# Kernel optimization log

Measured on AMD Instinct MI355X. Metric: run time of the kernel, lower is better.

Reference implementation:

```python
import jax, jax.numpy as jnp
import numpy as np

L, H, NH, V, T, B, K = 12, 768, 12, 30522, 512, 4, 21
DH = H // NH
INV_SQRT_DH = 1.0 / float(np.sqrt(DH))
NEG = -1e4  # BERT additive mask value
LN_EPS = 1e-12


def _ln(x, g, b):
    m = x.mean(-1, keepdims=True)
    v = jnp.var(x, axis=-1, keepdims=True)
    return (x - m) * jax.lax.rsqrt(v + LN_EPS) * g + b


def _encoder(input_ids, attention_mask, word_emb, pos_emb, tok_emb, emb_g, emb_b,
             Wqkv, bqkv, Wo, bo, ln1_g, ln1_b, W1, b1, W2, b2, ln2_g, ln2_b):
    Bv, Tv = input_ids.shape
    h = word_emb[input_ids] + pos_emb[None, :Tv] + tok_emb[0]  # token_type_ids = 0
    h = _ln(h, emb_g, emb_b)
    bias = (1.0 - attention_mask[:, None, None, :].astype(h.dtype)) * NEG  # [B,1,1,T]

    def layer(h, xs):
        wqkv, bq, wo, bo_, g1, b1_, w1, bb1, w2, bb2, g2, b2_ = xs
        qkv = h @ wqkv + bq  # [B,T,3H]
        q, k, v = jnp.split(qkv, 3, axis=-1)
        def hd(x):
            return x.reshape(Bv, Tv, NH, DH).transpose(0, 2, 1, 3)
        q, k, v = hd(q), hd(k), hd(v)
        scores = jnp.einsum('bhqd,bhkd->bhqk', q, k) * INV_SQRT_DH + bias
        ctx = jnp.einsum('bhqk,bhkd->bhqd', jax.nn.softmax(scores, axis=-1), v)
        ctx = ctx.transpose(0, 2, 1, 3).reshape(Bv, Tv, H)
        h = _ln(h + ctx @ wo + bo_, g1, b1_)  # post-LN (BERT)
        ff = jax.nn.gelu(h @ w1 + bb1, approximate=False) @ w2 + bb2
        h = _ln(h + ff, g2, b2_)
        return h, None

    h, _ = jax.lax.scan(layer, h, (Wqkv, bqkv, Wo, bo, ln1_g, ln1_b, W1, b1, W2, b2, ln2_g, ln2_b))
    return h


def _crf_nll(emissions, tags, mask, start, end, trans):
    # emissions [B,T,K], tags [B,T] int, mask [B,T] bool; torchcrf reduction='mean'
    Bv, Tv, Kv = emissions.shape
    maskf = mask.astype(emissions.dtype)
    # numerator: score of the gold path
    num = start[tags[:, 0]] + emissions[jnp.arange(Bv), 0, tags[:, 0]]
    em_t = jnp.take_along_axis(emissions, tags[..., None], axis=-1)[..., 0]  # [B,T]
    tr_t = trans[tags[:, :-1], tags[:, 1:]]  # [B,T-1]
    num = num + jnp.sum((tr_t + em_t[:, 1:]) * maskf[:, 1:], axis=1)
    last_idx = mask.sum(axis=1).astype(jnp.int32) - 1
    last_tag = jnp.take_along_axis(tags, last_idx[:, None], axis=1)[:, 0]
    num = num + end[last_tag]
    # denominator: forward algorithm (logsumexp recursion over time)
    alpha0 = start[None, :] + emissions[:, 0]  # [B,K]

    def step(alpha, xs):
        em, m = xs  # em [B,K], m [B] bool
        nxt = jax.scipy.special.logsumexp(alpha[:, :, None] + trans[None] + em[:, None, :], axis=1)
        return jnp.where(m[:, None], nxt, alpha), None

    alpha, _ = jax.lax.scan(step, alpha0, (emissions[:, 1:].transpose(1, 0, 2), mask[:, 1:].T))
    den = jax.scipy.special.logsumexp(alpha + end[None, :], axis=1)
    return -(num - den).mean()


def _viterbi(emissions, mask, start, end, trans):
    # Returns [B,T] int32 best paths; padded tail repeats the last valid tag.
    Bv, Tv, Kv = emissions.shape
    score0 = start[None, :] + emissions[:, 0]
    ident = jnp.broadcast_to(jnp.arange(Kv), (Bv, Kv))

    def step(score, xs):
        em, m = xs
        cand = score[:, :, None] + trans[None]  # [B,K_prev,K_next]
        idx = jnp.where(m[:, None], jnp.argmax(cand, axis=1), ident)
        nxt = jnp.max(cand, axis=1) + em
        return jnp.where(m[:, None], nxt, score), idx

    score, hist = jax.lax.scan(step, score0, (emissions[:, 1:].transpose(1, 0, 2), mask[:, 1:].T))
    last = jnp.argmax(score + end[None, :], axis=1)  # [B]

    def back(nxt_tag, idx):
        prev = jnp.take_along_axis(idx, nxt_tag[:, None], axis=1)[:, 0]
        return prev, nxt_tag

    tag0, rest = jax.lax.scan(back, last, hist, reverse=True)  # rest[i] = tag at t=i+1
    return jnp.concatenate([tag0[None], rest], axis=0).T.astype(jnp.int32)


def setup_inputs():
    key = jax.random.key(0)
    ks = jax.random.split(key, 16)
    s = 0.02

    def n(k, shape):
        return (s * jax.random.normal(k, shape)).astype(jnp.float32)

    def u(k, shape):
        return jax.random.uniform(k, shape, minval=-0.1, maxval=0.1).astype(jnp.float32)

    p = {}
    p['input_ids'] = jax.random.randint(ks[0], (B, T), 0, V)
    lengths = jax.random.randint(ks[1], (B,), T // 2, T + 1)
    p['attention_mask'] = (jnp.arange(T)[None, :] < lengths[:, None]).astype(jnp.int32)
    p['valid_mask'] = p['attention_mask']
    p['labels'] = jax.random.randint(ks[2], (B, T), 0, K)
    p['word_emb'] = n(ks[3], (V, H))
    p['pos_emb'] = n(ks[4], (T, H))
    p['tok_emb'] = n(ks[5], (2, H))
    p['emb_g'] = jnp.ones((H,), jnp.float32)
    p['emb_b'] = jnp.zeros((H,), jnp.float32)
    p['Wqkv'] = n(ks[6], (L, H, 3 * H))
    p['bqkv'] = jnp.zeros((L, 3 * H), jnp.float32)
    p['Wo'] = n(ks[7], (L, H, H))
    p['bo'] = jnp.zeros((L, H), jnp.float32)
    p['ln1_g'] = jnp.ones((L, H), jnp.float32)
    p['ln1_b'] = jnp.zeros((L, H), jnp.float32)
    p['W1'] = n(ks[8], (L, H, 4 * H))
    p['b1'] = jnp.zeros((L, 4 * H), jnp.float32)
    p['W2'] = n(ks[9], (L, 4 * H, H))
    p['b2'] = jnp.zeros((L, H), jnp.float32)
    p['ln2_g'] = jnp.ones((L, H), jnp.float32)
    p['ln2_b'] = jnp.zeros((L, H), jnp.float32)
    p['Wc'] = n(ks[10], (H, K))
    p['bc'] = jnp.zeros((K,), jnp.float32)
    p['crf_start'] = u(ks[11], (K,))
    p['crf_end'] = u(ks[12], (K,))
    p['crf_trans'] = u(ks[13], (K, K))
    return p


def reference(input_ids, attention_mask, valid_mask, labels,
              word_emb, pos_emb, tok_emb, emb_g, emb_b,
              Wqkv, bqkv, Wo, bo, ln1_g, ln1_b, W1, b1, W2, b2, ln2_g, ln2_b,
              Wc, bc, crf_start, crf_end, crf_trans):
    h = _encoder(input_ids, attention_mask, word_emb, pos_emb, tok_emb, emb_g, emb_b,
                 Wqkv, bqkv, Wo, bo, ln1_g, ln1_b, W1, b1, W2, b2, ln2_g, ln2_b)
    emissions = h @ Wc + bc  # dropout is identity in eval/reference mode
    mask = attention_mask.astype(bool)
    nll = _crf_nll(emissions, labels, mask, crf_start, crf_end, crf_trans)
    decoded = _viterbi(emissions, mask, crf_start, crf_end, crf_trans)
    return nll, decoded
```

## Files before the change

### kernel.cpp

```cpp
#include <hip/hip_runtime.h>
#include <math.h>

constexpr int NLAYER = 12;
constexpr int H = 768;
constexpr int NH = 12;
constexpr int DH = 64;
constexpr int T = 512;
constexpr int B = 4;
constexpr int K = 21;
constexpr int BT = B * T;
constexpr float NEGB = -10000.0f;
constexpr float LNEPS = 1e-12f;
constexpr float INV_SQRT_DH = 0.125f;

typedef __attribute__((ext_vector_type(8))) short bf16x8;
typedef __attribute__((ext_vector_type(4))) float f32x4;
typedef __attribute__((ext_vector_type(4))) unsigned short u16x4;

#define WAIT_VMCNT(n) asm volatile("s_waitcnt vmcnt(" #n ")")

__device__ __forceinline__ float wave_sum_f(float v) {
#pragma unroll
  for (int off = 32; off > 0; off >>= 1) v += __shfl_xor(v, off);
  return v;
}
__device__ __forceinline__ int wave_sum_i(int v) {
#pragma unroll
  for (int off = 32; off > 0; off >>= 1) v += __shfl_xor(v, off);
  return v;
}
__device__ __forceinline__ float readlane_f(float v, int i) {
  return __uint_as_float(__builtin_amdgcn_readlane(__float_as_uint(v), i));
}
__device__ __forceinline__ unsigned short f32_bf16_rn(float x) {
  unsigned int u = __float_as_uint(x);
  u += 0x7fffu + ((u >> 16) & 1u);
  return (unsigned short)(u >> 16);
}
__device__ __forceinline__ void split_bf16(float x, unsigned short& h, unsigned short& l) {
  h = f32_bf16_rn(x);
  float hf = __uint_as_float((unsigned int)h << 16);
  l = f32_bf16_rn(x - hf);
}
__device__ __forceinline__ void block_reduce_sum2(float& s, float& q) {
  __shared__ float red[8];
  s = wave_sum_f(s);
  q = wave_sum_f(q);
  int lane = threadIdx.x & 63, wid = threadIdx.x >> 6;
  if (lane == 0) { red[wid] = s; red[4 + wid] = q; }
  __syncthreads();
  s = red[0] + red[1] + red[2] + red[3];
  q = red[4] + red[5] + red[6] + red[7];
}

__global__ __launch_bounds__(256) void embed_ln_kernel(
    const int* __restrict__ ids, const float* __restrict__ wemb,
    const float* __restrict__ pemb, const float* __restrict__ temb,
    const float* __restrict__ g, const float* __restrict__ bta,
    float* __restrict__ h, unsigned short* __restrict__ hh,
    unsigned short* __restrict__ hl) {
  int row = blockIdx.x;
  int t = row % T;
  int id = ids[row];
  const float* wp = wemb + (size_t)id * H;
  const float* pp = pemb + (size_t)t * H;
  float x[3];
  float s = 0.f, q = 0.f;
#pragma unroll
  for (int i = 0; i < 3; i++) {
    int c = threadIdx.x + i * 256;
    x[i] = wp[c] + pp[c] + temb[c];
    s += x[i];
    q += x[i] * x[i];
  }
  block_reduce_sum2(s, q);
  float mean = s * (1.0f / H);
  float var = q * (1.0f / H) - mean * mean;
  float inv = rsqrtf(var + LNEPS);
#pragma unroll
  for (int i = 0; i < 3; i++) {
    int c = threadIdx.x + i * 256;
    float y = (x[i] - mean) * inv * g[c] + bta[c];
    h[(size_t)row * H + c] = y;
    unsigned short yh, yl;
    split_bf16(y, yh, yl);
    hh[(size_t)row * H + c] = yh;
    hl[(size_t)row * H + c] = yl;
  }
}

__global__ __launch_bounds__(256) void add_ln_kernel(
    float* __restrict__ h, const float* __restrict__ add,
    const float* __restrict__ g, const float* __restrict__ bta,
    unsigned short* __restrict__ hh, unsigned short* __restrict__ hl) {
  int row = blockIdx.x;
  size_t base = (size_t)row * H;
  float x[3];
  float s = 0.f, q = 0.f;
#pragma unroll
  for (int i = 0; i < 3; i++) {
    int c = threadIdx.x + i * 256;
    x[i] = h[base + c] + add[base + c];
    s += x[i];
    q += x[i] * x[i];
  }
  block_reduce_sum2(s, q);
  float mean = s * (1.0f / H);
  float var = q * (1.0f / H) - mean * mean;
  float inv = rsqrtf(var + LNEPS);
#pragma unroll
  for (int i = 0; i < 3; i++) {
    int c = threadIdx.x + i * 256;
    float y = (x[i] - mean) * inv * g[c] + bta[c];
    h[base + c] = y;
    unsigned short yh, yl;
    split_bf16(y, yh, yl);
    hh[base + c] = yh;
    hl[base + c] = yl;
  }
}

__global__ __launch_bounds__(256) void wconv_kernel(
    const float* __restrict__ w0, const float* __restrict__ w1,
    const float* __restrict__ w2, const float* __restrict__ w3,
    unsigned short* __restrict__ Wth, unsigned short* __restrict__ Wtl) {
  __shared__ float tile[32][33];
  int bid = blockIdx.x;
  const float* src;
  int Kd, N, tk, tn;
  size_t off;
  if (bid < 1728) {
    src = w0; Kd = 768; N = 2304; tk = bid / 72; tn = bid % 72; off = 0;
  } else if (bid < 2304) {
    int t2 = bid - 1728; src = w1; Kd = 768; N = 768; tk = t2 / 24; tn = t2 % 24;
    off = 1769472;
  } else if (bid < 4608) {
    int t2 = bid - 2304; src = w2; Kd = 768; N = 3072; tk = t2 / 96; tn = t2 % 96;
    off = 2359296;
  } else {
    int t2 = bid - 4608; src = w3; Kd = 3072; N = 768; tk = t2 / 24; tn = t2 % 24;
    off = 4718592;
  }
  int tid = threadIdx.x;
  int k0 = tk * 32, n0 = tn * 32;
  int r = tid >> 3, c = (tid & 7) * 4;
  float4 v = *(const float4*)(src + (size_t)(k0 + r) * N + n0 + c);
  tile[r][c + 0] = v.x; tile[r][c + 1] = v.y; tile[r][c + 2] = v.z; tile[r][c + 3] = v.w;
  __syncthreads();
  u16x4 hv, lv;
#pragma unroll
  for (int q2 = 0; q2 < 4; q2++) {
    unsigned short sh, sl;
    split_bf16(tile[c + q2][r], sh, sl);
    hv[q2] = sh; lv[q2] = sl;
  }
  size_t dst = off + (size_t)(n0 + r) * Kd + k0 + c;
  *(u16x4*)(Wth + dst) = hv;
  *(u16x4*)(Wtl + dst) = lv;
}

template <int BN, bool GELU, bool SPLITOUT>
__global__ __launch_bounds__(256) void gemm_bf3_kernel(
    const unsigned short* __restrict__ Ah, const unsigned short* __restrict__ Al,
    const unsigned short* __restrict__ Wth, const unsigned short* __restrict__ Wtl,
    const float* __restrict__ bias, float* __restrict__ C,
    unsigned short* __restrict__ Ch, unsigned short* __restrict__ Cl,
    int N, int Kd) {
  constexpr int WN = BN / 2;
  constexpr int FN = WN / 16;
  constexpr int AW = 128 * 32;
  constexpr int WW = BN * 32;
  constexpr int DBS = 2 * AW + 2 * WW;
  __shared__ short lds_s[2 * DBS];
  int tid = threadIdx.x;
  int lane = tid & 63, wid = tid >> 6;
  int wr = wid >> 1, wc = wid & 1;
  int bm = blockIdx.y * 128, bn = blockIdx.x * BN;
  f32x4 acc[4][FN] = {};
  int lrow = lane >> 2, lslot = lane & 3;

  const unsigned short* sbase;
  int rowbase, ldsoff, nchunks;
  if (wid == 0)      { sbase = Ah;  rowbase = bm; ldsoff = 0;            nchunks = 8; }
  else if (wid == 1) { sbase = Al;  rowbase = bm; ldsoff = AW;           nchunks = 8; }
  else if (wid == 2) { sbase = Wth; rowbase = bn; ldsoff = 2 * AW;       nchunks = BN / 16; }
  else               { sbase = Wtl; rowbase = bn; ldsoff = 2 * AW + WW;  nchunks = BN / 16; }

  const unsigned short* srcbase = sbase + (size_t)(rowbase + lrow) * Kd + lslot * 8;

  auto STAGE = [&](int db, int k0) {
#pragma unroll
    for (int c = 0; c < 8; c++) {
      if (c < nchunks) {
        const unsigned short* src = srcbase + (size_t)(c * 16) * Kd + k0;
        char* dst = ((char*)lds_s) + (db * DBS + ldsoff) * 2 + c * 1024 + lane * 16;
        __builtin_amdgcn_global_load_lds(
            (const __attribute__((address_space(1))) void*)src,
            (__attribute__((address_space(3))) void*)dst, 16, 0, 0);
      }
    }
  };

  const int NT = Kd / 32;
  STAGE(0, 0);
  for (int kt = 0; kt < NT; kt++) {
    int cur = kt & 1;
    bool more = (kt + 1 < NT);
    if (more) STAGE(cur ^ 1, (kt + 1) * 32);
    if (more) {
      if (BN == 128 || wid < 2) { WAIT_VMCNT(8); } else { WAIT_VMCNT(4); }
    } else {
      WAIT_VMCNT(0);
    }
    __builtin_amdgcn_s_barrier();
    __builtin_amdgcn_sched_barrier(0);

    int lr = lane & 15, lg = lane >> 4;
    int cb = cur * DBS;
    bf16x8 af_h[4], af_l[4], wf_h[FN], wf_l[FN];
#pragma unroll
    for (int i = 0; i < 4; i++) {
      int e = (wr * 64 + i * 16 + lr) * 32 + lg * 8;
      af_h[i] = *(const bf16x8*)&lds_s[cb + e];
      af_l[i] = *(const bf16x8*)&lds_s[cb + AW + e];
    }
#pragma unroll
    for (int j = 0; j < FN; j++) {
      int e = (wc * WN + j * 16 + lr) * 32 + lg * 8;
      wf_h[j] = *(const bf16x8*)&lds_s[cb + 2 * AW + e];
      wf_l[j] = *(const bf16x8*)&lds_s[cb + 2 * AW + WW + e];
    }
#pragma unroll
    for (int i = 0; i < 4; i++)
#pragma unroll
      for (int j = 0; j < FN; j++) {
        acc[i][j] = __builtin_amdgcn_mfma_f32_16x16x32_bf16(af_h[i], wf_h[j], acc[i][j], 0, 0, 0);
        acc[i][j] = __builtin_amdgcn_mfma_f32_16x16x32_bf16(af_l[i], wf_h[j], acc[i][j], 0, 0, 0);
        acc[i][j] = __builtin_amdgcn_mfma_f32_16x16x32_bf16(af_h[i], wf_l[j], acc[i][j], 0, 0, 0);
      }
    asm volatile("s_waitcnt lgkmcnt(0)");
    __builtin_amdgcn_sched_barrier(0);
    __builtin_amdgcn_s_barrier();
    __builtin_amdgcn_sched_barrier(0);
  }

  int lr = lane & 15, lg = lane >> 4;
#pragma unroll
  for (int i = 0; i < 4; i++) {
#pragma unroll
    for (int j = 0; j < FN; j++) {
      int row = bm + wr * 64 + i * 16 + lg * 4;
      int col = bn + wc * WN + j * 16 + lr;
      float bv = bias[col];
#pragma unroll
      for (int r = 0; r < 4; r++) {
        float v = acc[i][j][r] + bv;
        if (GELU) v = 0.5f * v * (1.0f + erff(v * 0.70710678118654752f));
        if (SPLITOUT) {
          unsigned short sh, sl;
          split_bf16(v, sh, sl);
          Ch[(size_t)(row + r) * N + col] = sh;
          Cl[(size_t)(row + r) * N + col] = sl;
        } else {
          C[(size_t)(row + r) * N + col] = v;
        }
      }
    }
  }
}

__global__ __launch_bounds__(256) void qk_kernel(
    const float* __restrict__ qkv, const int* __restrict__ mask,
    float* __restrict__ S) {
  int bh = blockIdx.z;
  int b = bh / NH, hh = bh % NH;
  int i0 = blockIdx.y * 64, j0 = blockIdx.x * 64;
  __shared__ float Qs[64][64];
  __shared__ float Ks[64][64];
  int tid = threadIdx.x;
  int r = tid >> 2;
  int cseg = (tid & 3) * 16;
  const float* qbase = qkv + (size_t)(b * T + i0 + r) * (3 * H) + hh * DH;
  const float* kbase = qkv + (size_t)(b * T + j0 + r) * (3 * H) + H + hh * DH;
#pragma unroll
  for (int ss = 0; ss < 4; ss++) {
    int c = cseg + ss * 4;
    float4 qa = *(const float4*)(qbase + c);
    float4 ka = *(const float4*)(kbase + c);
    Qs[c + 0][r] = qa.x; Qs[c + 1][r] = qa.y; Qs[c + 2][r] = qa.z; Qs[c + 3][r] = qa.w;
    Ks[c + 0][r] = ka.x; Ks[c + 1][r] = ka.y; Ks[c + 2][r] = ka.z; Ks[c + 3][r] = ka.w;
  }
  __syncthreads();
  int tx = tid & 15, ty = tid >> 4;
  float acc[4][4] = {};
#pragma unroll 4
  for (int d = 0; d < 64; d++) {
    float a_[4], b_[4];
    *(float4*)a_ = *(const float4*)&Qs[d][ty * 4];
    *(float4*)b_ = *(const float4*)&Ks[d][tx * 4];
#pragma unroll
    for (int i = 0; i < 4; i++)
#pragma unroll
      for (int j = 0; j < 4; j++)
        acc[i][j] = fmaf(a_[i], b_[j], acc[i][j]);
  }
  float bj[4];
#pragma unroll
  for (int q = 0; q < 4; q++)
    bj[q] = (1.0f - (float)mask[b * T + j0 + tx * 4 + q]) * NEGB;
#pragma unroll
  for (int i = 0; i < 4; i++) {
    int gi = i0 + ty * 4 + i;
    int gj = j0 + tx * 4;
    float4 o;
    o.x = acc[i][0] * INV_SQRT_DH + bj[0];
    o.y = acc[i][1] * INV_SQRT_DH + bj[1];
    o.z = acc[i][2] * INV_SQRT_DH + bj[2];
    o.w = acc[i][3] * INV_SQRT_DH + bj[3];
    *(float4*)(S + ((size_t)bh * T + gi) * T + gj) = o;
  }
}

__global__ __launch_bounds__(128) void softmax_kernel(float* __restrict__ S) {
  size_t row = blockIdx.x;
  float* p = S + row * T;
  int tid = threadIdx.x;
  float4 v = *(float4*)(p + tid * 4);
  float m = fmaxf(fmaxf(v.x, v.y), fmaxf(v.z, v.w));
#pragma unroll
  for (int off = 32; off > 0; off >>= 1) m = fmaxf(m, __shfl_xor(m, off));
  __shared__ float redm[2];
  __shared__ float reds[2];
  int wid = tid >> 6;
  if ((tid & 63) == 0) redm[wid] = m;
  __syncthreads();
  m = fmaxf(redm[0], redm[1]);
  v.x = __expf(v.x - m);
  v.y = __expf(v.y - m);
  v.z = __expf(v.z - m);
  v.w = __expf(v.w - m);
  float s = v.x + v.y + v.z + v.w;
  s = wave_sum_f(s);
  if ((tid & 63) == 0) reds[wid] = s;
  __syncthreads();
  s = reds[0] + reds[1];
  float inv = 1.0f / s;
  v.x *= inv; v.y *= inv; v.z *= inv; v.w *= inv;
  *(float4*)(p + tid * 4) = v;
}

__global__ __launch_bounds__(256) void pv_kernel(
    const float* __restrict__ S, const float* __restrict__ qkv,
    unsigned short* __restrict__ cth, unsigned short* __restrict__ ctl) {
  int bh = blockIdx.y;
  int b = bh / NH, hh = bh % NH;
  int i0 = blockIdx.x * 64;
  __shared__ float Ps[64][68];
  __shared__ float Vs[64][64];
  int tid = threadIdx.x;
  int r = tid >> 2;
  int cseg = (tid & 3) * 16;
  int tx = tid & 15, ty = tid >> 4;
  float acc[4][4] = {};
  const float* srow = S + ((size_t)bh * T + i0 + r) * T;
  const float* vbase = qkv + (size_t)(b * T) * (3 * H) + 2 * H + hh * DH;
  for (int k0 = 0; k0 < T; k0 += 64) {
    __syncthreads();
#pragma unroll
    for (int ss = 0; ss < 4; ss++) {
      int c = cseg + ss * 4;
      *(float4*)&Ps[r][c] = *(const float4*)(srow + k0 + c);
      *(float4*)&Vs[r][c] = *(const float4*)(vbase + (size_t)(k0 + r) * (3 * H) + c);
    }
    __syncthreads();
#pragma unroll
    for (int kk = 0; kk < 64; kk += 4) {
      float p_[4][4], v_[4][4];
#pragma unroll
      for (int i = 0; i < 4; i++)
        *(float4*)p_[i] = *(const float4*)&Ps[ty * 4 + i][kk];
#pragma unroll
      for (int s = 0; s < 4; s++)
        *(float4*)v_[s] = *(const float4*)&Vs[kk + s][tx * 4];
#pragma unroll
      for (int i = 0; i < 4; i++)
#pragma unroll
        for (int s = 0; s < 4; s++)
#pragma unroll
          for (int j = 0; j < 4; j++)
            acc[i][j] = fmaf(p_[i][s], v_[s][j], acc[i][j]);
    }
  }
#pragma unroll
  for (int i = 0; i < 4; i++) {
    int gi = i0 + ty * 4 + i;
    size_t idx = (size_t)(b * T + gi) * H + hh * DH + tx * 4;
    u16x4 hv, lv;
#pragma unroll
    for (int j = 0; j < 4; j++) {
      unsigned short sh, sl;
      split_bf16(acc[i][j], sh, sl);
      hv[j] = sh; lv[j] = sl;
    }
    *(u16x4*)(cth + idx) = hv;
    *(u16x4*)(ctl + idx) = lv;
  }
}

__global__ __launch_bounds__(256) void classifier_kernel(
    const float* __restrict__ h, const float* __restrict__ Wc,
    const float* __restrict__ bc, float* __restrict__ em) {
  int id = blockIdx.x * 256 + threadIdx.x;
  if (id >= BT * K) return;
  int row = id / K, k = id % K;
  float acc = bc[k];
  const float* hr = h + (size_t)row * H;
  for (int d = 0; d < H; d++) acc = fmaf(hr[d], Wc[d * K + k], acc);
  em[id] = acc;
}

#define MRG(vo, io, va, ia, vb, ib) \
  float vo = ((vb) > (va)) ? (vb) : (va); \
  int io = ((vb) > (va)) ? (ib) : (ia);

__global__ __launch_bounds__(64) void crf_fused_kernel(
    const float* __restrict__ em, const int* __restrict__ labels,
    const int* __restrict__ mask, const float* __restrict__ start,
    const float* __restrict__ endv, const float* __restrict__ trans,
    float* __restrict__ parts, float* __restrict__ outdec) {
  __shared__ float em_s[T * K];
  __shared__ int mask_s[T];
  __shared__ unsigned char hist_s[(T - 1) * K];
  __shared__ float sc_s[32];
  int b = blockIdx.x & 3;
  int role = blockIdx.x >> 2;
  int j = threadIdx.x;
  const float* eb = em + (size_t)b * T * K;
  for (int i = j; i < T * K / 4; i += 64)
    ((float4*)em_s)[i] = ((const float4*)eb)[i];
  for (int i = j; i < T; i += 64) mask_s[i] = mask[b * T + i];
  __syncthreads();
  bool act = (j < K);
  float tr[K];
#pragma unroll
  for (int i = 0; i < K; i++) tr[i] = act ? trans[i * K + j] : 0.f;

  if (role == 0) {
    const int* tb = labels + b * T;
    float numloc = 0.f;
    int cnt = 0;
    for (int t = j; t < T; t += 64) {
      cnt += mask_s[t];
      if (t >= 1 && mask_s[t]) {
        int tp = tb[t - 1], tc = tb[t];
        numloc += trans[tp * K + tc] + em_s[t * K + tc];
      }
    }
    float num = wave_sum_f(numloc);
    int cnttot = wave_sum_i(cnt);
    float etr[K];
#pragma unroll
    for (int i = 0; i < K; i++) etr[i] = __expf(tr[i]);
    float alpha = act ? (start[j] + em_s[j]) : 0.f;
    for (int t = 1; t < T; t++) {
      if (!mask_s[t]) continue;
      float m0 = readlane_f(alpha, 0);
      float ee = __expf(alpha - m0);
      float e0 = readlane_f(ee, 0),  e1 = readlane_f(ee, 1),  e2 = readlane_f(ee, 2);
      float e3 = readlane_f(ee, 3),  e4 = readlane_f(ee, 4),  e5 = readlane_f(ee, 5);
      float e6 = readlane_f(ee, 6),  e7 = readlane_f(ee, 7),  e8 = readlane_f(ee, 8);
      float e9 = readlane_f(ee, 9),  e10 = readlane_f(ee, 10), e11 = readlane_f(ee, 11);
      float e12 = readlane_f(ee, 12), e13 = readlane_f(ee, 13), e14 = readlane_f(ee, 14);
      float e15 = readlane_f(ee, 15), e16 = readlane_f(ee, 16), e17 = readlane_f(ee, 17);
      float e18 = readlane_f(ee, 18), e19 = readlane_f(ee, 19), e20 = readlane_f(ee, 20);
      float a0 = fmaf(e16, etr[16], fmaf(e12, etr[12], fmaf(e8, etr[8],  fmaf(e4, etr[4], e0 * etr[0]))));
      float a1 = fmaf(e17, etr[17], fmaf(e13, etr[13], fmaf(e9, etr[9],  fmaf(e5, etr[5], e1 * etr[1]))));
      float a2 = fmaf(e18, etr[18], fmaf(e14, etr[14], fmaf(e10, etr[10], fmaf(e6, etr[6], e2 * etr[2]))));
      float a3 = fmaf(e19, etr[19], fmaf(e15, etr[15], fmaf(e11, etr[11], fmaf(e7, etr[7], e3 * etr[3]))));
      float ssum = fmaf(e20, etr[20], (a0 + a1) + (a2 + a3));
      float nxt = __logf(ssum) + m0 + (act ? em_s[t * K + j] : 0.f);
      if (act) alpha = nxt;
    }
    float aj = act ? (alpha + endv[j]) : -3.0e38f;
    float mm = aj;
#pragma unroll
    for (int off = 32; off > 0; off >>= 1) mm = fmaxf(mm, __shfl_xor(mm, off));
    float e2v = act ? __expf(aj - mm) : 0.f;
    float s2 = wave_sum_f(e2v);
    float den = __logf(s2) + mm;
    if (j == 0) {
      int tag0 = tb[0];
      int lastidx = cnttot - 1;
      float numtot = num + start[tag0] + em_s[tag0] + endv[tb[lastidx]];
      parts[b] = numtot - den;
    }
  } else {
    float score = act ? (start[j] + em_s[j]) : 0.f;
    for (int t = 1; t < T; t++) {
      int mk = mask_s[t];
      if (mk) {
        float c0 = readlane_f(score, 0) + tr[0],   c1 = readlane_f(score, 1) + tr[1];
        float c2 = readlane_f(score, 2) + tr[2],   c3 = readlane_f(score, 3) + tr[3];
        float c4 = readlane_f(score, 4) + tr[4],   c5 = readlane_f(score, 5) + tr[5];
        float c6 = readlane_f(score, 6) + tr[6],   c7 = readlane_f(score, 7) + tr[7];
        float c8 = readlane_f(score, 8) + tr[8],   c9 = readlane_f(score, 9) + tr[9];
        float c10 = readlane_f(score, 10) + tr[10], c11 = readlane_f(score, 11) + tr[11];
        float c12 = readlane_f(score, 12) + tr[12], c13 = readlane_f(score, 13) + tr[13];
        float c14 = readlane_f(score, 14) + tr[14], c15 = readlane_f(score, 15) + tr[15];
        float c16 = readlane_f(score, 16) + tr[16], c17 = readlane_f(score, 17) + tr[17];
        float c18 = readlane_f(score, 18) + tr[18], c19 = readlane_f(score, 19) + tr[19];
        float c20 = readlane_f(score, 20) + tr[20];
        MRG(m0v, m0i, c0, 0, c1, 1)
        MRG(m1v, m1i, c2, 2, c3, 3)
        MRG(m2v, m2i, c4, 4, c5, 5)
        MRG(m3v, m3i, c6, 6, c7, 7)
        MRG(m4v, m4i, c8, 8, c9, 9)
        MRG(m5v, m5i, c10, 10, c11, 11)
        MRG(m6v, m6i, c12, 12, c13, 13)
        MRG(m7v, m7i, c14, 14, c15, 15)
        MRG(m8v, m8i, c16, 16, c17, 17)
        MRG(m9v, m9i, c18, 18, c19, 19)
        MRG(p0v, p0i, m0v, m0i, m1v, m1i)
        MRG(p1v, p1i, m2v, m2i, m3v, m3i)
        MRG(p2v, p2i, m4v, m4i, m5v, m5i)
        MRG(p3v, p3i, m6v, m6i, m7v, m7i)
        MRG(p4v, p4i, m8v, m8i, m9v, m9i)
        MRG(r0v, r0i, p0v, p0i, p1v, p1i)
        MRG(r1v, r1i, p2v, p2i, p3v, p3i)
        MRG(r2v, r2i, p4v, p4i, c20, 20)
        MRG(s0v, s0i, r0v, r0i, r1v, r1i)
        MRG(fv, fi, s0v, s0i, r2v, r2i)
        if (act) {
          hist_s[(t - 1) * K + j] = (unsigned char)fi;
          score = fv + em_s[t * K + j];
        }
      } else if (act) {
        hist_s[(t - 1) * K + j] = (unsigned char)j;
      }
    }
    if (act) sc_s[j] = score + endv[j];
    __syncthreads();
    if (j == 0) {
      float best = -3.0e38f;
      int cur = 0;
#pragma unroll
      for (int i = 0; i < K; i++)
        if (sc_s[i] > best) { best = sc_s[i]; cur = i; }
      outdec[b * T + (T - 1)] = (float)cur;
      for (int t = T - 1; t >= 1; t--) {
        cur = hist_s[(t - 1) * K + cur];
        outdec[b * T + (t - 1)] = (float)cur;
      }
    }
  }
}

__global__ void nll_final_kernel(const float* __restrict__ parts,
                                 float* __restrict__ out) {
  out[0] = -0.25f * (parts[0] + parts[1] + parts[2] + parts[3]);
}

extern "C" void kernel_launch(void* const* d_in, const int* in_sizes, int n_in,
                              void* d_out, int out_size, void* d_ws, size_t ws_size,
                              hipStream_t stream) {
  (void)in_sizes; (void)n_in; (void)out_size; (void)ws_size;
  const int* ids    = (const int*)d_in[0];
  const int* amask  = (const int*)d_in[1];
  const int* labels = (const int*)d_in[3];
  const float* wemb = (const float*)d_in[4];
  const float* pemb = (const float*)d_in[5];
  const float* temb = (const float*)d_in[6];
  const float* eg   = (const float*)d_in[7];
  const float* ebta = (const float*)d_in[8];
  const float* Wqkv = (const float*)d_in[9];
  const float* bqkv = (const float*)d_in[10];
  const float* Wo   = (const float*)d_in[11];
  const float* bo   = (const float*)d_in[12];
  const float* ln1g = (const float*)d_in[13];
  const float* ln1b = (const float*)d_in[14];
  const float* W1   = (const float*)d_in[15];
  const float* b1   = (const float*)d_in[16];
  const float* W2   = (const float*)d_in[17];
  const float* b2   = (const float*)d_in[18];
  const float* ln2g = (const float*)d_in[19];
  const float* ln2b = (const float*)d_in[20];
  const float* Wc   = (const float*)d_in[21];
  const float* bc   = (const float*)d_in[22];
  const float* cst  = (const float*)d_in[23];
  const float* cen  = (const float*)d_in[24];
  const float* ctr  = (const float*)d_in[25];
  float* out = (float*)d_out;

  float* ws = (float*)d_ws;
  float* h    = ws;
  unsigned short* hh = (unsigned short*)(h + 1572864);
  unsigned short* hl = (unsigned short*)(h + 1572864 + 786432);
  float* qkv  = h + 1572864 + 786432 * 2;
  unsigned short* cth = (unsigned short*)(qkv + 4718592);
  unsigned short* ctl = (unsigned short*)(qkv + 4718592 + 786432);
  float* tmp  = qkv + 4718592 + 786432 * 2;
  float* big  = tmp + 1572864;
  unsigned short* gh = (unsigned short*)(big + 12582912);
  unsigned short* gl = (unsigned short*)(big + 12582912 + 3145728);
  unsigned short* Wth = (unsigned short*)(big + 12582912 + 3145728 * 2);
  unsigned short* Wtl = (unsigned short*)(big + 12582912 + 3145728 * 2 + 3538944);
  float* em   = big + 12582912 + 3145728 * 2 + 3538944 * 2;
  float* parts = em + 43008;

  embed_ln_kernel<<<BT, 256, 0, stream>>>(ids, wemb, pemb, temb, eg, ebta, h, hh, hl);

  for (int l = 0; l < NLAYER; l++) {
    const float* bqkv_l = bqkv + (size_t)l * 3 * H;
    const float* bo_l   = bo + (size_t)l * H;
    const float* b1_l   = b1 + (size_t)l * 4 * H;
    const float* b2_l   = b2 + (size_t)l * H;

    wconv_kernel<<<6912, 256, 0, stream>>>(
        Wqkv + (size_t)l * H * 3 * H, Wo + (size_t)l * H * H,
        W1 + (size_t)l * H * 4 * H, W2 + (size_t)l * 4 * H * H, Wth, Wtl);

    gemm_bf3_kernel<128, false, false><<<dim3(18, 16), 256, 0, stream>>>(
        hh, hl, Wth, Wtl, bqkv_l, qkv, nullptr, nullptr, 3 * H, H);
    qk_kernel<<<dim3(T / 64, T / 64, B * NH), 256, 0, stream>>>(qkv, amask, big);
    softmax_kernel<<<B * NH * T, 128, 0, stream>>>(big);
    pv_kernel<<<dim3(T / 64, B * NH), 256, 0, stream>>>(big, qkv, cth, ctl);
    gemm_bf3_kernel<64, false, false><<<dim3(12, 16), 256, 0, stream>>>(
        cth, ctl, Wth + 1769472, Wtl + 1769472, bo_l, tmp, nullptr, nullptr, H, H);
    add_ln_kernel<<<BT, 256, 0, stream>>>(h, tmp, ln1g + (size_t)l * H, ln1b + (size_t)l * H, hh, hl);
    gemm_bf3_kernel<128, true, true><<<dim3(24, 16), 256, 0, stream>>>(
        hh, hl, Wth + 2359296, Wtl + 2359296, b1_l, nullptr, gh, gl, 4 * H, H);
    gemm_bf3_kernel<64, false, false><<<dim3(12, 16), 256, 0, stream>>>(
        gh, gl, Wth + 4718592, Wtl + 4718592, b2_l, tmp, nullptr, nullptr, H, 4 * H);
    add_ln_kernel<<<BT, 256, 0, stream>>>(h, tmp, ln2g + (size_t)l * H, ln2b + (size_t)l * H, hh, hl);
  }

  classifier_kernel<<<(BT * K + 255) / 256, 256, 0, stream>>>(h, Wc, bc, em);
  crf_fused_kernel<<<8, 64, 0, stream>>>(em, labels, amask, cst, cen, ctr, parts, out + 1);
  nll_final_kernel<<<1, 1, 0, stream>>>(parts, out);
}
```

Measured before the change: 3.354 ms.

## Swizzle GEMM LDS layout and bound CRF recursions by mask length

The bf16x3 GEMM now XOR-swizzles the 16-byte slot within each 64-byte LDS row, both when staging with global_load_lds and when reading fragments. This is meant to cut LDS bank conflicts on the fragment reads. The CRF forward and Viterbi loops now run only up to the mask length and prefetch the next emission from LDS, and backtracking fills the padded tail with the last tag. That shortcut assumes the mask is a contiguous prefix, which holds for BERT-style masks but is not checked.

Result: faster. 3.251 ms (-3.1%).

```diff
diff --git a/kernel.cpp b/kernel.cpp
--- a/kernel.cpp
+++ b/kernel.cpp
@@ -177,7 +177,8 @@
   int wr = wid >> 1, wc = wid & 1;
   int bm = blockIdx.y * 128, bn = blockIdx.x * BN;
   f32x4 acc[4][FN] = {};
-  int lrow = lane >> 2, lslot = lane & 3;
+  int lrow = lane >> 2;
+  int lslot_sw = (lane & 3) ^ ((lrow >> 1) & 3);
 
   const unsigned short* sbase;
   int rowbase, ldsoff, nchunks;
@@ -186,7 +187,7 @@
   else if (wid == 2) { sbase = Wth; rowbase = bn; ldsoff = 2 * AW;       nchunks = BN / 16; }
   else               { sbase = Wtl; rowbase = bn; ldsoff = 2 * AW + WW;  nchunks = BN / 16; }
 
-  const unsigned short* srcbase = sbase + (size_t)(rowbase + lrow) * Kd + lslot * 8;
+  const unsigned short* srcbase = sbase + (size_t)(rowbase + lrow) * Kd + lslot_sw * 8;
 
   auto STAGE = [&](int db, int k0) {
 #pragma unroll
@@ -216,17 +217,18 @@
     __builtin_amdgcn_sched_barrier(0);
 
     int lr = lane & 15, lg = lane >> 4;
+    int slot = (lg ^ ((lr >> 1) & 3)) * 8;
     int cb = cur * DBS;
     bf16x8 af_h[4], af_l[4], wf_h[FN], wf_l[FN];
 #pragma unroll
     for (int i = 0; i < 4; i++) {
-      int e = (wr * 64 + i * 16 + lr) * 32 + lg * 8;
+      int e = (wr * 64 + i * 16 + lr) * 32 + slot;
       af_h[i] = *(const bf16x8*)&lds_s[cb + e];
       af_l[i] = *(const bf16x8*)&lds_s[cb + AW + e];
     }
 #pragma unroll
     for (int j = 0; j < FN; j++) {
-      int e = (wc * WN + j * 16 + lr) * 32 + lg * 8;
+      int e = (wc * WN + j * 16 + lr) * 32 + slot;
       wf_h[j] = *(const bf16x8*)&lds_s[cb + 2 * AW + e];
       wf_l[j] = *(const bf16x8*)&lds_s[cb + 2 * AW + WW + e];
     }
@@ -445,25 +447,27 @@
 #pragma unroll
   for (int i = 0; i < K; i++) tr[i] = act ? trans[i * K + j] : 0.f;
 
+  int cntloc = 0;
+  for (int t = j; t < T; t += 64) cntloc += mask_s[t];
+  int cnt = wave_sum_i(cntloc);
+
   if (role == 0) {
     const int* tb = labels + b * T;
     float numloc = 0.f;
-    int cnt = 0;
     for (int t = j; t < T; t += 64) {
-      cnt += mask_s[t];
       if (t >= 1 && mask_s[t]) {
         int tp = tb[t - 1], tc = tb[t];
         numloc += trans[tp * K + tc] + em_s[t * K + tc];
       }
     }
     float num = wave_sum_f(numloc);
-    int cnttot = wave_sum_i(cnt);
     float etr[K];
 #pragma unroll
     for (int i = 0; i < K; i++) etr[i] = __expf(tr[i]);
     float alpha = act ? (start[j] + em_s[j]) : 0.f;
-    for (int t = 1; t < T; t++) {
-      if (!mask_s[t]) continue;
+    float emv = act ? em_s[K + j] : 0.f;
+    for (int t = 1; t < cnt; t++) {
+      float emv_n = (act && (t + 1) < cnt) ? em_s[(t + 1) * K + j] : 0.f;
       float m0 = readlane_f(alpha, 0);
       float ee = __expf(alpha - m0);
       float e0 = readlane_f(ee, 0),  e1 = readlane_f(ee, 1),  e2 = readlane_f(ee, 2);
@@ -478,8 +482,9 @@
       float a2 = fmaf(e18, etr[18], fmaf(e14, etr[14], fmaf(e10, etr[10], fmaf(e6, etr[6], e2 * etr[2]))));
       float a3 = fmaf(e19, etr[19], fmaf(e15, etr[15], fmaf(e11, etr[11], fmaf(e7, etr[7], e3 * etr[3]))));
       float ssum = fmaf(e20, etr[20], (a0 + a1) + (a2 + a3));
-      float nxt = __logf(ssum) + m0 + (act ? em_s[t * K + j] : 0.f);
+      float nxt = __logf(ssum) + m0 + emv;
       if (act) alpha = nxt;
+      emv = emv_n;
     }
     float aj = act ? (alpha + endv[j]) : -3.0e38f;
     float mm = aj;
@@ -490,64 +495,62 @@
     float den = __logf(s2) + mm;
     if (j == 0) {
       int tag0 = tb[0];
-      int lastidx = cnttot - 1;
-      float numtot = num + start[tag0] + em_s[tag0] + endv[tb[lastidx]];
+      float numtot = num + start[tag0] + em_s[tag0] + endv[tb[cnt - 1]];
       parts[b] = numtot - den;
     }
   } else {
     float score = act ? (start[j] + em_s[j]) : 0.f;
-    for (int t = 1; t < T; t++) {
-      int mk = mask_s[t];
-      if (mk) {
-        float c0 = readlane_f(score, 0) + tr[0],   c1 = readlane_f(score, 1) + tr[1];
-        float c2 = readlane_f(score, 2) + tr[2],   c3 = readlane_f(score, 3) + tr[3];
-        float c4 = readlane_f(score, 4) + tr[4],   c5 = readlane_f(score, 5) + tr[5];
-        float c6 = readlane_f(score, 6) + tr[6],   c7 = readlane_f(score, 7) + tr[7];
-        float c8 = readlane_f(score, 8) + tr[8],   c9 = readlane_f(score, 9) + tr[9];
-        float c10 = readlane_f(score, 10) + tr[10], c11 = readlane_f(score, 11) + tr[11];
-        float c12 = readlane_f(score, 12) + tr[12], c13 = readlane_f(score, 13) + tr[13];
-        float c14 = readlane_f(score, 14) + tr[14], c15 = readlane_f(score, 15) + tr[15];
-        float c16 = readlane_f(score, 16) + tr[16], c17 = readlane_f(score, 17) + tr[17];
-        float c18 = readlane_f(score, 18) + tr[18], c19 = readlane_f(score, 19) + tr[19];
-        float c20 = readlane_f(score, 20) + tr[20];
-        MRG(m0v, m0i, c0, 0, c1, 1)
-        MRG(m1v, m1i, c2, 2, c3, 3)
-        MRG(m2v, m2i, c4, 4, c5, 5)
-        MRG(m3v, m3i, c6, 6, c7, 7)
-        MRG(m4v, m4i, c8, 8, c9, 9)
-        MRG(m5v, m5i, c10, 10, c11, 11)
-        MRG(m6v, m6i, c12, 12, c13, 13)
-        MRG(m7v, m7i, c14, 14, c15, 15)
-        MRG(m8v, m8i, c16, 16, c17, 17)
-        MRG(m9v, m9i, c18, 18, c19, 19)
-        MRG(p0v, p0i, m0v, m0i, m1v, m1i)
-        MRG(p1v, p1i, m2v, m2i, m3v, m3i)
-        MRG(p2v, p2i, m4v, m4i, m5v, m5i)
-        MRG(p3v, p3i, m6v, m6i, m7v, m7i)
-        MRG(p4v, p4i, m8v, m8i, m9v, m9i)
-        MRG(r0v, r0i, p0v, p0i, p1v, p1i)
-        MRG(r1v, r1i, p2v, p2i, p3v, p3i)
-        MRG(r2v, r2i, p4v, p4i, c20, 20)
-        MRG(s0v, s0i, r0v, r0i, r1v, r1i)
-        MRG(fv, fi, s0v, s0i, r2v, r2i)
-        if (act) {
-          hist_s[(t - 1) * K + j] = (unsigned char)fi;
-          score = fv + em_s[t * K + j];
-        }
-      } else if (act) {
-        hist_s[(t - 1) * K + j] = (unsigned char)j;
+    float emv = act ? em_s[K + j] : 0.f;
+    for (int t = 1; t < cnt; t++) {
+      float emv_n = (act && (t + 1) < cnt) ? em_s[(t + 1) * K + j] : 0.f;
+      float c0 = readlane_f(score, 0) + tr[0],   c1 = readlane_f(score, 1) + tr[1];
+      float c2 = readlane_f(score, 2) + tr[2],   c3 = readlane_f(score, 3) + tr[3];
+      float c4 = readlane_f(score, 4) + tr[4],   c5 = readlane_f(score, 5) + tr[5];
+      float c6 = readlane_f(score, 6) + tr[6],   c7 = readlane_f(score, 7) + tr[7];
+      float c8 = readlane_f(score, 8) + tr[8],   c9 = readlane_f(score, 9) + tr[9];
+      float c10 = readlane_f(score, 10) + tr[10], c11 = readlane_f(score, 11) + tr[11];
+      float c12 = readlane_f(score, 12) + tr[12], c13 = readlane_f(score, 13) + tr[13];
+      float c14 = readlane_f(score, 14) + tr[14], c15 = readlane_f(score, 15) + tr[15];
+      float c16 = readlane_f(score, 16) + tr[16], c17 = readlane_f(score, 17) + tr[17];
+      float c18 = readlane_f(score, 18) + tr[18], c19 = readlane_f(score, 19) + tr[19];
+      float c20 = readlane_f(score, 20) + tr[20];
+      MRG(m0v, m0i, c0, 0, c1, 1)
+      MRG(m1v, m1i, c2, 2, c3, 3)
+      MRG(m2v, m2i, c4, 4, c5, 5)
+      MRG(m3v, m3i, c6, 6, c7, 7)
+      MRG(m4v, m4i, c8, 8, c9, 9)
+      MRG(m5v, m5i, c10, 10, c11, 11)
+      MRG(m6v, m6i, c12, 12, c13, 13)
+      MRG(m7v, m7i, c14, 14, c15, 15)
+      MRG(m8v, m8i, c16, 16, c17, 17)
+      MRG(m9v, m9i, c18, 18, c19, 19)
+      MRG(p0v, p0i, m0v, m0i, m1v, m1i)
+      MRG(p1v, p1i, m2v, m2i, m3v, m3i)
+      MRG(p2v, p2i, m4v, m4i, m5v, m5i)
+      MRG(p3v, p3i, m6v, m6i, m7v, m7i)
+      MRG(p4v, p4i, m8v, m8i, m9v, m9i)
+      MRG(r0v, r0i, p0v, p0i, p1v, p1i)
+      MRG(r1v, r1i, p2v, p2i, p3v, p3i)
+      MRG(r2v, r2i, p4v, p4i, c20, 20)
+      MRG(s0v, s0i, r0v, r0i, r1v, r1i)
+      MRG(fv, fi, s0v, s0i, r2v, r2i)
+      if (act) {
+        hist_s[(t - 1) * K + j] = (unsigned char)fi;
+        score = fv + emv;
       }
+      emv = emv_n;
     }
     if (act) sc_s[j] = score + endv[j];
     __syncthreads();
     if (j == 0) {
       float best = -3.0e38f;
-      int cur = 0;
+      int last = 0;
 #pragma unroll
       for (int i = 0; i < K; i++)
-        if (sc_s[i] > best) { best = sc_s[i]; cur = i; }
-      outdec[b * T + (T - 1)] = (float)cur;
-      for (int t = T - 1; t >= 1; t--) {
+        if (sc_s[i] > best) { best = sc_s[i]; last = i; }
+      for (int t = cnt - 1; t < T; t++) outdec[b * T + t] = (float)last;
+      int cur = last;
+      for (int t = cnt - 1; t >= 1; t--) {
         cur = hist_s[(t - 1) * K + cur];
         outdec[b * T + (t - 1)] = (float)cur;
       }
```
